# Kernel tuning notes

Hardware: AMD Instinct MI355X
Metric: run time of the kernel (lower is better)

Reference implementation:

```python
import jax, jax.numpy as jnp
import numpy as np

B, N, D = 8192, 49, 3
D3 = 42  # embed_dim // 3
E = 128
K = 3    # min(3, N-1) nearest neighbors for local density


def setup_inputs() -> dict:
    key = jax.random.key(0)
    ks = jax.random.split(key, 8)
    points = jax.random.normal(ks[0], (B, N, D), jnp.float32)
    return {
        "points": points,
        "W_dist": jax.random.normal(ks[1], (1, D3), jnp.float32) * 1.0,
        "b_dist": jnp.zeros((D3,), jnp.float32),
        "emb": jax.random.normal(ks[2], (50, D3), jnp.float32) * 0.02,
        "W_den": jax.random.normal(ks[3], (1, D3), jnp.float32) * 1.0,
        "b_den": jnp.zeros((D3,), jnp.float32),
        "W_out": jax.random.normal(ks[4], (3 * D3, E), jnp.float32) * (1.0 / np.sqrt(3 * D3)),
        "b_out": jnp.zeros((E,), jnp.float32),
    }


def _local_density(points):
    # Batched cdist with diagonal masked to +inf, then mean of K smallest dists.
    sq = jnp.sum(points * points, axis=-1)                      # [B,N]
    d2 = sq[:, :, None] + sq[:, None, :] \
         - 2.0 * jnp.einsum('bnd,bmd->bnm', points, points)      # [B,N,N]
    d2 = jnp.maximum(d2, 0.0)
    eye = jnp.eye(points.shape[1], dtype=bool)
    d2 = jnp.where(eye, jnp.inf, d2)
    dists = jnp.sqrt(d2)
    nearest = -jax.lax.top_k(-dists, K)[0]                      # [B,N,K] smallest
    return jnp.mean(nearest, axis=-1, keepdims=True)            # [B,N,1]


def reference(points, W_dist, b_dist, emb, W_den, b_den, W_out, b_out):
    b, n, _ = points.shape
    centroid = jnp.mean(points, axis=1, keepdims=True)          # [B,1,3]
    rel = points - centroid
    centroid_dist = jnp.linalg.norm(rel, axis=-1, keepdims=True)  # [B,N,1]
    dist_f = centroid_dist @ W_dist + b_dist                    # [B,N,D3]
    # n_valid == N (no mask), a constant index into the count embedding
    count_f = jnp.broadcast_to(emb[n][None, None, :], (b, n, emb.shape[1]))
    density = _local_density(points)                            # [B,N,1]
    den_f = density @ W_den + b_den                             # [B,N,D3]
    features = jnp.concatenate([dist_f, count_f, den_f], axis=-1)  # [B,N,3*D3]
    return features @ W_out + b_out                             # [B,N,E]
```

## Files before the change

### kernel.cpp

```cpp
#include <hip/hip_runtime.h>
#include <math.h>

#define N_   49
#define D3_  42
#define E_   128


__global__ void precompute_uvc(const float* __restrict__ W_dist,
                               const float* __restrict__ b_dist,
                               const float* __restrict__ emb,
                               const float* __restrict__ W_den,
                               const float* __restrict__ b_den,
                               const float* __restrict__ W_out,
                               const float* __restrict__ b_out,
                               float* __restrict__ uvc) {
    int e = threadIdx.x;
    if (e >= E_) return;
    const float* embN = emb + N_ * D3_;
    float u = 0.f, v = 0.f, c = b_out[e];
    for (int j = 0; j < D3_; ++j) {
        float w0 = W_out[j * E_ + e];
        float w1 = W_out[(D3_ + j) * E_ + e];
        float w2 = W_out[(2 * D3_ + j) * E_ + e];
        u = fmaf(W_dist[j], w0, u);
        v = fmaf(W_den[j], w2, v);
        c = fmaf(b_dist[j], w0, c);
        c = fmaf(embN[j], w1, c);
        c = fmaf(b_den[j], w2, c);
    }
    uvc[e]          = u;
    uvc[E_ + e]     = v;
    uvc[2 * E_ + e] = c;
}

__global__ __launch_bounds__(64) void compute_cdden(
        const float* __restrict__ points,
        float2* __restrict__ cdden) {
    __shared__ float pts[N_ * 3];
    const int tid = threadIdx.x;
    const long long b = blockIdx.x;
    const float* pb = points + b * (N_ * 3);

    for (int i = tid; i < N_ * 3; i += 64) pts[i] = pb[i];
    __syncthreads();

    if (tid < N_) {
        const float px = pts[3 * tid], py = pts[3 * tid + 1], pz = pts[3 * tid + 2];
        float sx = 0.f, sy = 0.f, sz = 0.f;
        float s0 = INFINITY, s1 = INFINITY, s2 = INFINITY;
        for (int m = 0; m < N_; ++m) {
            float qx = pts[3 * m], qy = pts[3 * m + 1], qz = pts[3 * m + 2];
            sx += qx; sy += qy; sz += qz;
            float dx = px - qx, dy = py - qy, dz = pz - qz;
            float d2 = fmaf(dx, dx, fmaf(dy, dy, dz * dz));
            if (m != tid) {
                if (d2 < s0)      { s2 = s1; s1 = s0; s0 = d2; }
                else if (d2 < s1) { s2 = s1; s1 = d2; }
                else if (d2 < s2) { s2 = d2; }
            }
        }
        const float inv = 1.0f / (float)N_;
        float cx = sx * inv, cy = sy * inv, cz = sz * inv;
        float dx = px - cx, dy = py - cy, dz = pz - cz;
        float cd  = sqrtf(fmaf(dx, dx, fmaf(dy, dy, dz * dz)));
        float den = (sqrtf(s0) + sqrtf(s1) + sqrtf(s2)) * (1.0f / 3.0f);
        cdden[b * N_ + tid] = make_float2(cd, den);
    }
}

__global__ __launch_bounds__(256) void rank2_write(
        const float2* __restrict__ cdden,
        const float4* __restrict__ uvc4,
        float4* __restrict__ out4,
        int total_rows) {
    const int q   = threadIdx.x & 31;
    const int sub = threadIdx.x >> 5;
    const float4 u = uvc4[q];
    const float4 v = uvc4[32 + q];
    const float4 c = uvc4[64 + q];
    const long long stride = (long long)gridDim.x * 8;
    for (long long r = (long long)blockIdx.x * 8 + sub; r < total_rows; r += stride) {
        float2 ad = cdden[r];
        float4 w;
        w.x = fmaf(ad.x, u.x, fmaf(ad.y, v.x, c.x));
        w.y = fmaf(ad.x, u.y, fmaf(ad.y, v.y, c.y));
        w.z = fmaf(ad.x, u.z, fmaf(ad.y, v.z, c.z));
        w.w = fmaf(ad.x, u.w, fmaf(ad.y, v.w, c.w));
        out4[r * 32 + q] = w;
    }
}

extern "C" void kernel_launch(void* const* d_in, const int* in_sizes, int n_in,
                              void* d_out, int out_size, void* d_ws, size_t ws_size,
                              hipStream_t stream) {
    const float* points = (const float*)d_in[0];
    const float* W_dist = (const float*)d_in[1];
    const float* b_dist = (const float*)d_in[2];
    const float* emb    = (const float*)d_in[3];
    const float* W_den  = (const float*)d_in[4];
    const float* b_den  = (const float*)d_in[5];
    const float* W_out  = (const float*)d_in[6];
    const float* b_out  = (const float*)d_in[7];

    float*  uvc   = (float*)d_ws;
    float2* cdden = (float2*)((char*)d_ws + 1536);

    const int B = in_sizes[0] / (N_ * 3);
    const int total_rows = B * N_;

    precompute_uvc<<<1, 128, 0, stream>>>(W_dist, b_dist, emb, W_den, b_den,
                                          W_out, b_out, uvc);
    compute_cdden<<<B, 64, 0, stream>>>(points, cdden);
    rank2_write<<<4096, 256, 0, stream>>>(cdden, (const float4*)uvc,
                                          (float4*)d_out, total_rows);
}
```

Measured before the change: 238.5 us.

## Fuse density computation and rank-2 output write into one per-wave kernel

Merges the per-batch centroid-distance and k-nearest density kernel with the output expansion kernel. Each 64-lane wave now handles one batch: it computes the (cd, den) pairs into shared memory and immediately writes that batch's 49x128 output rows. This removes the intermediate global cdden buffer round-trip and one kernel launch. It relies on wave-synchronous shared-memory visibility instead of a __syncthreads barrier, which carries some correctness risk.

```diff
diff --git a/kernel.cpp b/kernel.cpp
--- a/kernel.cpp
+++ b/kernel.cpp
@@ -4,7 +4,7 @@
 #define N_   49
 #define D3_  42
 #define E_   128
-
+#define WAVES_PER_BLOCK 4
 
 __global__ void precompute_uvc(const float* __restrict__ W_dist,
                                const float* __restrict__ b_dist,
@@ -33,27 +33,38 @@
     uvc[2 * E_ + e] = c;
 }
 
-__global__ __launch_bounds__(64) void compute_cdden(
+__global__ __launch_bounds__(256) void fused_rank2(
         const float* __restrict__ points,
-        float2* __restrict__ cdden) {
-    __shared__ float pts[N_ * 3];
-    const int tid = threadIdx.x;
-    const long long b = blockIdx.x;
+        const float4* __restrict__ uvc4,
+        float4* __restrict__ out4,
+        int B) {
+    __shared__ float  pts[WAVES_PER_BLOCK][N_ * 3];
+    __shared__ float2 cdden[WAVES_PER_BLOCK][N_];
+
+    const int lane = threadIdx.x & 63;
+    const int w    = threadIdx.x >> 6;
+    const long long b = (long long)blockIdx.x * WAVES_PER_BLOCK + w;
+    if (b >= B) return;
+
+    const int q = lane & 31;
+    const float4 u = uvc4[q];
+    const float4 v = uvc4[32 + q];
+    const float4 c = uvc4[64 + q];
+
     const float* pb = points + b * (N_ * 3);
+    for (int i = lane; i < N_ * 3; i += 64) pts[w][i] = pb[i];
 
-    for (int i = tid; i < N_ * 3; i += 64) pts[i] = pb[i];
-    __syncthreads();
-
-    if (tid < N_) {
-        const float px = pts[3 * tid], py = pts[3 * tid + 1], pz = pts[3 * tid + 2];
+    if (lane < N_) {
+        const float px = pts[w][3 * lane], py = pts[w][3 * lane + 1],
+                    pz = pts[w][3 * lane + 2];
         float sx = 0.f, sy = 0.f, sz = 0.f;
         float s0 = INFINITY, s1 = INFINITY, s2 = INFINITY;
         for (int m = 0; m < N_; ++m) {
-            float qx = pts[3 * m], qy = pts[3 * m + 1], qz = pts[3 * m + 2];
+            float qx = pts[w][3 * m], qy = pts[w][3 * m + 1], qz = pts[w][3 * m + 2];
             sx += qx; sy += qy; sz += qz;
             float dx = px - qx, dy = py - qy, dz = pz - qz;
             float d2 = fmaf(dx, dx, fmaf(dy, dy, dz * dz));
-            if (m != tid) {
+            if (m != lane) {
                 if (d2 < s0)      { s2 = s1; s1 = s0; s0 = d2; }
                 else if (d2 < s1) { s2 = s1; s1 = d2; }
                 else if (d2 < s2) { s2 = d2; }
@@ -64,29 +75,23 @@
         float dx = px - cx, dy = py - cy, dz = pz - cz;
         float cd  = sqrtf(fmaf(dx, dx, fmaf(dy, dy, dz * dz)));
         float den = (sqrtf(s0) + sqrtf(s1) + sqrtf(s2)) * (1.0f / 3.0f);
-        cdden[b * N_ + tid] = make_float2(cd, den);
+        cdden[w][lane] = make_float2(cd, den);
     }
-}
 
-__global__ __launch_bounds__(256) void rank2_write(
-        const float2* __restrict__ cdden,
-        const float4* __restrict__ uvc4,
-        float4* __restrict__ out4,
-        int total_rows) {
-    const int q   = threadIdx.x & 31;
-    const int sub = threadIdx.x >> 5;
-    const float4 u = uvc4[q];
-    const float4 v = uvc4[32 + q];
-    const float4 c = uvc4[64 + q];
-    const long long stride = (long long)gridDim.x * 8;
-    for (long long r = (long long)blockIdx.x * 8 + sub; r < total_rows; r += stride) {
-        float2 ad = cdden[r];
-        float4 w;
-        w.x = fmaf(ad.x, u.x, fmaf(ad.y, v.x, c.x));
-        w.y = fmaf(ad.x, u.y, fmaf(ad.y, v.y, c.y));
-        w.z = fmaf(ad.x, u.z, fmaf(ad.y, v.z, c.z));
-        w.w = fmaf(ad.x, u.w, fmaf(ad.y, v.w, c.w));
-        out4[r * 32 + q] = w;
+    float4* ob = out4 + b * (long long)(N_ * 32);
+    #pragma unroll 5
+    for (int j = 0; j < 25; ++j) {
+        int g = j * 64 + lane;
+        if (g < N_ * 32) {
+            int row = g >> 5;
+            float2 ad = cdden[w][row];
+            float4 r;
+            r.x = fmaf(ad.x, u.x, fmaf(ad.y, v.x, c.x));
+            r.y = fmaf(ad.x, u.y, fmaf(ad.y, v.y, c.y));
+            r.z = fmaf(ad.x, u.z, fmaf(ad.y, v.z, c.z));
+            r.w = fmaf(ad.x, u.w, fmaf(ad.y, v.w, c.w));
+            ob[g] = r;
+        }
     }
 }
 
@@ -102,15 +107,13 @@
     const float* W_out  = (const float*)d_in[6];
     const float* b_out  = (const float*)d_in[7];
 
-    float*  uvc   = (float*)d_ws;
-    float2* cdden = (float2*)((char*)d_ws + 1536);
+    float* uvc = (float*)d_ws;
 
     const int B = in_sizes[0] / (N_ * 3);
-    const int total_rows = B * N_;
+    const int nblocks = (B + WAVES_PER_BLOCK - 1) / WAVES_PER_BLOCK;
 
     precompute_uvc<<<1, 128, 0, stream>>>(W_dist, b_dist, emb, W_den, b_den,
                                           W_out, b_out, uvc);
-    compute_cdden<<<B, 64, 0, stream>>>(points, cdden);
-    rank2_write<<<4096, 256, 0, stream>>>(cdden, (const float4*)uvc,
-                                          (float4*)d_out, total_rows);
+    fused_rank2<<<nblocks, 64 * WAVES_PER_BLOCK, 0, stream>>>(
+        points, (const float4*)uvc, (float4*)d_out, B);
 }
```

New measurement: 228.5 us. -4.2%, faster.
